# Kernel optimization log

Measured on AMD Instinct MI355X. Metric: run time of the kernel, lower is better.

## Reference

```python
import jax, jax.numpy as jnp
import numpy as np

B_SZ, L_SEQ, D_DATA = 2, 1024, 8
D_CTRL = 256
POLY = 40
N_LAYERS = 2
D_STATE = 16
D_CONV = 4
D_INNER = 1 * D_CTRL          # expand_factor_control = 1
DT_RANK = -(-D_CTRL // 16)    # ceil(d_model/16) = 16
EPS = 1e-5


def setup_inputs() -> dict:
    key = jax.random.key(0)
    ks = jax.random.split(key, 12)
    s = 0.02
    x = jax.random.uniform(ks[0], (B_SZ, L_SEQ, D_DATA), dtype=jnp.float32)
    y = jax.random.uniform(ks[1], (B_SZ, L_SEQ, D_DATA), dtype=jnp.float32)
    return {
        'x': x,
        'y': y,
        # control_proj (note: fed 2*d_data features in structured forward)
        'control_proj_w': jax.random.normal(ks[2], (D_CTRL, 2 * D_DATA)) * s,
        'control_proj_b': jnp.zeros((D_CTRL,), jnp.float32),
        # stacked Mamba layer params (leading dim = n_layers)
        'norm_w': jnp.ones((N_LAYERS, D_CTRL), jnp.float32),
        'in_proj_w': jax.random.normal(ks[3], (N_LAYERS, 2 * D_INNER, D_CTRL)) * s,
        'conv_w': jax.random.normal(ks[4], (N_LAYERS, D_INNER, D_CONV)) * s,
        'conv_b': jnp.zeros((N_LAYERS, D_INNER), jnp.float32),
        'x_proj_w': jax.random.normal(ks[5], (N_LAYERS, DT_RANK + 2 * D_STATE, D_INNER)) * s,
        'dt_proj_w': jax.random.normal(ks[6], (N_LAYERS, D_INNER, DT_RANK)) * s,
        'dt_proj_b': jnp.zeros((N_LAYERS, D_INNER), jnp.float32),
        'A_log': jnp.tile(jnp.log(jnp.arange(1, D_STATE + 1, dtype=jnp.float32))[None, None, :], (N_LAYERS, D_INNER, 1)),
        'D_skip': jnp.ones((N_LAYERS, D_INNER), jnp.float32),
        'out_proj_w': jax.random.normal(ks[7], (N_LAYERS, D_CTRL, D_INNER)) * s,
        # b_net: Linear(d_control, 2*d_data*poly_dim^2)
        'b_net_w': jax.random.normal(ks[8], (2 * D_DATA * POLY * POLY, D_CTRL)) * s,
        'b_net_b': jnp.zeros((2 * D_DATA * POLY * POLY,), jnp.float32),
    }


def _rmsnorm(u, w):
    return u * jax.lax.rsqrt(jnp.mean(u * u, axis=-1, keepdims=True) + EPS) * w


def _causal_conv(u, w, b):
    # u: [B,L,C]; w: [C,K] depthwise causal conv, pad left K-1
    K = w.shape[-1]
    L = u.shape[1]
    up = jnp.pad(u, ((0, 0), (K - 1, 0), (0, 0)))
    acc = jnp.zeros_like(u)
    for k in range(K):  # K=4, fixed small kernel
        acc = acc + up[:, k:k + L, :] * w[:, k]
    return acc + b


def _mamba(u, norm_w, in_proj_w, conv_w, conv_b, x_proj_w, dt_proj_w, dt_proj_b, A_log, D_skip, out_proj_w):
    # mambapy-style stack of residual blocks: u = mixer(rmsnorm(u)) + u
    for i in range(N_LAYERS):
        r = _rmsnorm(u, norm_w[i])
        xz = jnp.einsum('bld,ed->ble', r, in_proj_w[i])          # [B,L,2*di]
        xc, zg = jnp.split(xz, 2, axis=-1)
        xc = jax.nn.silu(_causal_conv(xc, conv_w[i], conv_b[i]))  # [B,L,di]
        dbc = jnp.einsum('bld,ed->ble', xc, x_proj_w[i])          # [B,L,dt_rank+2*ds]
        delta = jax.nn.softplus(jnp.einsum('blr,dr->bld', dbc[..., :DT_RANK], dt_proj_w[i]) + dt_proj_b[i])
        Bm = dbc[..., DT_RANK:DT_RANK + D_STATE]
        Cm = dbc[..., DT_RANK + D_STATE:]
        A = -jnp.exp(A_log[i])                                    # [di,ds]
        dA = jnp.exp(delta[..., None] * A)                        # [B,L,di,ds]
        dBx = delta[..., None] * Bm[:, :, None, :] * xc[..., None]

        def step(h, inp):
            dA_t, dBx_t = inp
            h = dA_t * h + dBx_t
            return h, h

        h0 = jnp.zeros((u.shape[0], D_INNER, D_STATE), u.dtype)
        _, hs = jax.lax.scan(step, h0, (dA.transpose(1, 0, 2, 3), dBx.transpose(1, 0, 2, 3)))
        yv = jnp.einsum('lbds,lbs->bld', hs, Cm.transpose(1, 0, 2)) + D_skip[i] * xc
        yv = yv * jax.nn.silu(zg)
        u = jnp.einsum('bld,ed->ble', yv, out_proj_w[i]) + u
    return u


def _power_mat(z):
    # z ** arange(POLY), built with cumprod (grad-safe at exponent 0)
    ones = jnp.ones(z.shape + (1,), z.dtype)
    reps = jnp.broadcast_to(z[..., None], z.shape + (POLY - 1,))
    return jnp.cumprod(jnp.concatenate([ones, reps], axis=-1), axis=-1)  # [B,L,2d,P]


def reference(x, y, control_proj_w, control_proj_b, norm_w, in_proj_w, conv_w, conv_b,
              x_proj_w, dt_proj_w, dt_proj_b, A_log, D_skip, out_proj_w, b_net_w, b_net_b):
    B, L, d = x.shape
    xdot = y - x
    z = jnp.concatenate([x, xdot], axis=-1)                       # [B,L,2d]
    pm = _power_mat(z)                                            # [B,L,2d,P]
    ctrl_in = jnp.flip(jnp.concatenate([xdot, y], axis=-1), axis=1)
    ctrl_in = ctrl_in @ control_proj_w.T + control_proj_b
    sp = _mamba(ctrl_in, norm_w, in_proj_w, conv_w, conv_b, x_proj_w,
                dt_proj_w, dt_proj_b, A_log, D_skip, out_proj_w)
    state_pred = jnp.flip(sp, axis=1)                             # [B,L,d_ctrl]
    bmat = (state_pred @ b_net_w.T + b_net_b).reshape(B, L, 2 * d, POLY, POLY)
    pow1 = jnp.einsum('bldkj,bldk->bldj', bmat, pm)
    zdot = jnp.einsum('bldj,bldj->bld', pow1, jnp.flip(pm, axis=2))
    return zdot[:, 1:, :], state_pred
```

## Files before the change

kernel.cpp:

```cpp
#include <hip/hip_runtime.h>
#include <hip/hip_bf16.h>

#define B_SZ   2
#define LSEQ   1024
#define DD     8
#define DCTRL  256
#define POLY   40
#define NL     2
#define DSTATE 16
#define DCONV  4
#define DINNER 256
#define DTRANK 16
#define NBL    (B_SZ*LSEQ)
#define NROWS  (2*DD*POLY*POLY)
#define NSLOT  25
#define NCH    32
#define LCH    32

typedef __attribute__((ext_vector_type(8))) short bf16x8;
typedef __attribute__((ext_vector_type(8))) unsigned short us8;
typedef __attribute__((ext_vector_type(4))) unsigned short us4;
typedef __attribute__((ext_vector_type(4))) float f32x4;

__device__ __forceinline__ float sigmoidf_(float x){ return 1.f/(1.f+__expf(-x)); }
__device__ __forceinline__ float softplusf_(float x){ return fmaxf(x,0.f) + log1pf(__expf(-fabsf(x))); }
__device__ __forceinline__ unsigned short f2bf(float f){
  unsigned int u = __float_as_uint(f);
  unsigned int r = (u + 0x7fffu + ((u>>16)&1u)) >> 16;
  return (unsigned short)r;
}

__global__ void k_f2bf(const float* __restrict__ in, unsigned short* __restrict__ out, int n8){
  int i = blockIdx.x*blockDim.x + threadIdx.x;
  if (i>=n8) return;
  const float4* p = (const float4*)(in + (size_t)i*8);
  float4 a = p[0], b = p[1];
  us8 r;
  r[0]=f2bf(a.x); r[1]=f2bf(a.y); r[2]=f2bf(a.z); r[3]=f2bf(a.w);
  r[4]=f2bf(b.x); r[5]=f2bf(b.y); r[6]=f2bf(b.z); r[7]=f2bf(b.w);
  *(us8*)(out + (size_t)i*8) = r;
}

#define IPW_N8 (NL*512*256/8)
#define OPW_N8 (NL*256*256/8)
#define PRE_B0 ((IPW_N8+OPW_N8)/256)
#define PRE_B1 (NL*288*256/256)
#define PRE_B2 (16*NBL/256)
#define PRE_B3 (NBL*256/256)
#define PRE_B4 (NROWS*256/8/256)
__global__ void k_prologue(const float* __restrict__ ipw, const float* __restrict__ opw,
                           const float* __restrict__ dtw, const float* __restrict__ xpw,
                           const float* __restrict__ x,   const float* __restrict__ y,
                           const float* __restrict__ cpw, const float* __restrict__ cpb,
                           const float* __restrict__ bnw,
                           unsigned short* __restrict__ ipwb,
                           unsigned short* __restrict__ wcomb,
                           float* __restrict__ pmt, float* __restrict__ u,
                           unsigned short* __restrict__ Wb){
  int bx = blockIdx.x; int tid = threadIdx.x;
  if (bx < PRE_B0){
    int i = bx*256 + tid;
    const float* src = (i < IPW_N8) ? (ipw + (size_t)i*8) : (opw + (size_t)(i-IPW_N8)*8);
    const float4* p = (const float4*)src;
    float4 a = p[0], b = p[1];
    us8 r;
    r[0]=f2bf(a.x); r[1]=f2bf(a.y); r[2]=f2bf(a.z); r[3]=f2bf(a.w);
    r[4]=f2bf(b.x); r[5]=f2bf(b.y); r[6]=f2bf(b.z); r[7]=f2bf(b.w);
    *(us8*)(ipwb + (size_t)i*8) = r;
  } else if (bx < PRE_B0+PRE_B1){
    int idx = (bx-PRE_B0)*256 + tid;
    int e = idx & 255; int row = (idx>>8) % 288; int l = idx / (288*256);
    float v;
    if (row < 256){
      float s=0.f;
      #pragma unroll
      for (int r=0;r<16;++r) s += dtw[((size_t)l*256+row)*16+r] * xpw[((size_t)l*48+r)*256+e];
      v = s;
    } else {
      v = xpw[((size_t)l*48 + (row-240))*256 + e];
    }
    wcomb[idx] = f2bf(v);
  } else if (bx < PRE_B0+PRE_B1+PRE_B2){
    int idx = (bx-PRE_B0-PRE_B1)*256 + tid;
    int m = idx & (NBL-1); int c = idx >> 11;
    float z;
    if (c < 8) z = x[(size_t)m*8 + c];
    else       z = y[(size_t)m*8 + (c-8)] - x[(size_t)m*8 + (c-8)];
    float p = 1.f;
    #pragma unroll
    for (int j=0;j<POLY;++j){ pmt[((size_t)c*POLY+j)*NBL + m] = p; p*=z; }
  } else if (bx < PRE_B0+PRE_B1+PRE_B2+PRE_B3){
    int idx = (bx-PRE_B0-PRE_B1-PRE_B2)*256 + tid;
    int e = idx & 255; int m = idx >> 8;
    int bb = m >> 10; int lm = m & 1023; int lo = 1023 - lm;
    const float* xp = x + ((size_t)bb*1024+lo)*8;
    const float* yp = y + ((size_t)bb*1024+lo)*8;
    const float* wr = cpw + (size_t)e*16;
    float acc = cpb[e];
    #pragma unroll
    for (int d=0; d<8; ++d) acc += (yp[d]-xp[d])*wr[d];
    #pragma unroll
    for (int d=0; d<8; ++d) acc += yp[d]*wr[8+d];
    u[idx] = acc;
  } else {
    int i = (bx-PRE_B0-PRE_B1-PRE_B2-PRE_B3)*256 + tid;
    const float4* p = (const float4*)(bnw + (size_t)i*8);
    float4 a = p[0], b = p[1];
    us8 r;
    r[0]=f2bf(a.x); r[1]=f2bf(a.y); r[2]=f2bf(a.z); r[3]=f2bf(a.w);
    r[4]=f2bf(b.x); r[5]=f2bf(b.y); r[6]=f2bf(b.z); r[7]=f2bf(b.w);
    *(us8*)(Wb + (size_t)i*8) = r;
  }
}

__global__ void k_rms(const float* __restrict__ u, const float* __restrict__ nw,
                      unsigned short* __restrict__ rb){
  int m = blockIdx.x; int e = threadIdx.x;
  float v = u[(size_t)m*256 + e];
  float ss = v*v;
  #pragma unroll
  for (int off=32; off>0; off>>=1) ss += __shfl_down(ss, off);
  __shared__ float sred[4];
  __shared__ float srstd;
  int wid = e>>6; int lane = e&63;
  if (lane==0) sred[wid]=ss;
  __syncthreads();
  if (e==0){ float t = sred[0]+sred[1]+sred[2]+sred[3]; srstd = rsqrtf(t*(1.f/256.f) + 1e-5f); }
  __syncthreads();
  rb[(size_t)m*256+e] = f2bf(v * srstd * nw[e]);
}

__global__ void __launch_bounds__(256)
gemm_bf(const unsigned short* __restrict__ A, const unsigned short* __restrict__ B,
        int N, int K, const float* __restrict__ bias,
        float* __restrict__ C0, float* __restrict__ C1, int ldc, int mode,
        float* __restrict__ outsp, unsigned short* __restrict__ spb){
  __shared__ __align__(16) unsigned short Asm[64*40];
  __shared__ __align__(16) unsigned short Bsm[64*40];
  int tid = threadIdx.x;
  int lane = tid & 63;
  int w = tid >> 6; int wr = w >> 1, wc = w & 1;
  int l15 = lane & 15, l4 = lane >> 4;
  int m0 = blockIdx.y*64, n0 = blockIdx.x*64;

  f32x4 acc[2][2];
  #pragma unroll
  for (int i=0;i<2;++i)
    #pragma unroll
    for (int j=0;j<2;++j){ acc[i][j][0]=0.f; acc[i][j][1]=0.f; acc[i][j][2]=0.f; acc[i][j][3]=0.f; }

  int row = tid>>2, c8 = tid&3;
  int nks = K >> 5;
  for (int ks=0; ks<nks; ++ks){
    int k0 = ks*32;
    *(us8*)&Asm[row*40 + c8*8] = *(const us8*)(A + (size_t)(m0+row)*K + k0 + c8*8);
    {
      int bn = n0+row;
      us8 v;
      if (bn < N){
        v = *(const us8*)(B + (size_t)bn*K + k0 + c8*8);
      } else {
        for (int z=0;z<8;++z) v[z]=0;
      }
      *(us8*)&Bsm[row*40 + c8*8] = v;
    }
    __syncthreads();
    bf16x8 av[2], bv[2];
    #pragma unroll
    for (int i=0;i<2;++i) av[i] = *(bf16x8*)&Asm[(wr*32+i*16+l15)*40 + l4*8];
    #pragma unroll
    for (int j=0;j<2;++j) bv[j] = *(bf16x8*)&Bsm[(wc*32+j*16+l15)*40 + l4*8];
    #pragma unroll
    for (int i=0;i<2;++i)
      #pragma unroll
      for (int j=0;j<2;++j)
        acc[i][j] = __builtin_amdgcn_mfma_f32_16x16x32_bf16(av[i], bv[j], acc[i][j], 0,0,0);
    __syncthreads();
  }

  #pragma unroll
  for (int i=0;i<2;++i){
    #pragma unroll
    for (int j=0;j<2;++j){
      int n = n0 + wc*32 + j*16 + l15;
      #pragma unroll
      for (int q=0;q<4;++q){
        int m = m0 + wr*32 + i*16 + l4*4 + q;
        float v = acc[i][j][q];
        if (mode==0){
          C0[(size_t)m*ldc + n] = v;
        } else if (mode==1){
          C0[(size_t)m*ldc + n] += v;
        } else if (mode==2){
          if (n < 256) C0[(size_t)m*256 + n] = softplusf_(v + bias[n]);
          else if (n < N) C1[(size_t)m*32 + (n-256)] = v;
        } else {
          float t = C0[(size_t)m*ldc + n] + v;
          int bb = m >> 10; int lq = m & 1023;
          size_t mf = (size_t)bb*1024 + (1023-lq);
          outsp[mf*256 + n] = t;
          spb[mf*256 + n] = f2bf(t);
        }
      }
    }
  }
}

__global__ void k_convsilu(const float* __restrict__ xz, const float* __restrict__ cw,
                           const float* __restrict__ cb, float* __restrict__ xc,
                           unsigned short* __restrict__ xcb){
  int idx = blockIdx.x*blockDim.x + threadIdx.x;
  if (idx >= NBL*64) return;
  int d4 = (idx & 63) << 2; int m = idx >> 6;
  int bb = m>>10, l = m&1023;
  float4 w0 = *(const float4*)&cw[(d4+0)*4];
  float4 w1 = *(const float4*)&cw[(d4+1)*4];
  float4 w2 = *(const float4*)&cw[(d4+2)*4];
  float4 w3 = *(const float4*)&cw[(d4+3)*4];
  float4 cbv = *(const float4*)&cb[d4];
  float a0=cbv.x, a1=cbv.y, a2=cbv.z, a3=cbv.w;
  #pragma unroll
  for (int k=0;k<4;++k){
    int ls = l - 3 + k;
    if (ls >= 0){
      float4 v = *(const float4*)&xz[((size_t)(bb*1024+ls))*512 + d4];
      a0 += v.x * ((const float*)&w0)[k];
      a1 += v.y * ((const float*)&w1)[k];
      a2 += v.z * ((const float*)&w2)[k];
      a3 += v.w * ((const float*)&w3)[k];
    }
  }
  a0 = a0*sigmoidf_(a0); a1 = a1*sigmoidf_(a1);
  a2 = a2*sigmoidf_(a2); a3 = a3*sigmoidf_(a3);
  float4 o; o.x=a0; o.y=a1; o.z=a2; o.w=a3;
  *(float4*)&xc[(size_t)m*256 + d4] = o;
  us4 ob; ob[0]=f2bf(a0); ob[1]=f2bf(a1); ob[2]=f2bf(a2); ob[3]=f2bf(a3);
  *(us4*)&xcb[(size_t)m*256 + d4] = ob;
}

__global__ void k_scan1(const float* __restrict__ delta, const float* __restrict__ bc,
                        const float* __restrict__ xc, const float* __restrict__ alog,
                        float* __restrict__ hend, float* __restrict__ Pc){
  int blk = blockIdx.x;
  int dg = blk & 15; int ch = (blk>>4) & (NCH-1); int bb = blk >> 9;
  int tid = threadIdx.x; int dl = tid>>4; int s = tid&15; int d = dg*16+dl;
  float A = -__expf(alog[(size_t)d*16+s]);
  float h = 0.f, p = 1.f;
  size_t base = (size_t)bb*1024 + ch*LCH;
  #pragma unroll 4
  for (int t=0;t<LCH;++t){
    size_t mb = base + t;
    float de  = delta[mb*256+d];
    float Bv  = bc[mb*32+s];
    float xcv = xc[mb*256+d];
    float a = __expf(de*A);
    h = a*h + de*Bv*xcv;
    p *= a;
  }
  size_t o = (((size_t)bb*NCH+ch)*256+d)*16+s;
  hend[o]=h; Pc[o]=p;
}

__global__ void k_scan2(const float* __restrict__ hend, const float* __restrict__ Pc,
                        float* __restrict__ Hinit){
  int idx = blockIdx.x*blockDim.x + threadIdx.x;
  if (idx >= B_SZ*256*16) return;
  int bb = idx >> 12; int ds = idx & 4095;
  float H = 0.f;
  #pragma unroll
  for (int ch=0; ch<NCH; ++ch){
    size_t o = ((size_t)bb*NCH+ch)*4096 + ds;
    Hinit[o] = H;
    H = Pc[o]*H + hend[o];
  }
}

__global__ void k_scan3(const float* __restrict__ delta, const float* __restrict__ bc,
                        const float* __restrict__ xc, const float* __restrict__ xz,
                        const float* __restrict__ alog, const float* __restrict__ dskip,
                        const float* __restrict__ Hinit, unsigned short* __restrict__ yvb){
  int blk = blockIdx.x;
  int dg = blk & 15; int ch = (blk>>4) & (NCH-1); int bb = blk >> 9;
  int tid = threadIdx.x; int dl = tid>>4; int s = tid&15; int d = dg*16+dl;
  float A = -__expf(alog[(size_t)d*16+s]);
  float dsk = dskip[d];
  float h = Hinit[(((size_t)bb*NCH+ch)*256+d)*16+s];
  size_t base = (size_t)bb*1024 + ch*LCH;
  #pragma unroll 2
  for (int t=0;t<LCH;++t){
    size_t mb = base + t;
    float de  = delta[mb*256+d];
    float Bv  = bc[mb*32+s];
    float Cv  = bc[mb*32+16+s];
    float xcv = xc[mb*256+d];
    float a = __expf(de*A);
    h = a*h + de*Bv*xcv;
    float yval = h*Cv;
    yval += __shfl_xor(yval,1);
    yval += __shfl_xor(yval,2);
    yval += __shfl_xor(yval,4);
    yval += __shfl_xor(yval,8);
    if (s==0){
      float zg = xz[mb*512+256+d];
      yvb[mb*256+d] = f2bf((yval + dsk*xcv) * zg * sigmoidf_(zg));
    }
  }
}

__global__ void __launch_bounds__(512)
k_bnet_mfma(const unsigned short* __restrict__ spb, const unsigned short* __restrict__ Wb,
            const float* __restrict__ bnb, const float* __restrict__ pmt,
            float* __restrict__ part){
  __shared__ __align__(16) unsigned short Asm[2][256*40];
  __shared__ __align__(16) unsigned short Bsm[2][64*40];
  __shared__ float red[2][256];

  int tid = threadIdx.x;
  int lane = tid & 63;
  int w = tid >> 6;
  int wr = w >> 1, wc = w & 1;
  int l15 = lane & 15, l4 = lane >> 4;
  int bx = blockIdx.x;
  int m0 = blockIdx.y*256;
  int n0 = bx*64;

  int aRow0 = (tid)>>2,        aC0 = (tid)&3;
  int aRow1 = (tid+512)>>2,    aC1 = (tid+512)&3;
  int bRow  = tid>>2,          bC  = tid&3;
  const unsigned short* aSrc0 = spb + ((size_t)(m0+aRow0))*256 + aC0*8;
  const unsigned short* aSrc1 = spb + ((size_t)(m0+aRow1))*256 + aC1*8;
  const unsigned short* bSrc  = Wb  + ((size_t)(n0+bRow ))*256 + bC*8;

  f32x4 acc[4][2];
  #pragma unroll
  for (int i=0;i<4;++i)
    #pragma unroll
    for (int j=0;j<2;++j){ acc[i][j][0]=0.f; acc[i][j][1]=0.f; acc[i][j][2]=0.f; acc[i][j][3]=0.f; }

  us8 rA0 = *(const us8*)(aSrc0);
  us8 rA1 = *(const us8*)(aSrc1);
  us8 rB;
  if (tid < 256) rB = *(const us8*)(bSrc);
  *(us8*)&Asm[0][aRow0*40 + aC0*8] = rA0;
  *(us8*)&Asm[0][aRow1*40 + aC1*8] = rA1;
  if (tid < 256) *(us8*)&Bsm[0][bRow*40 + bC*8] = rB;
  __syncthreads();

  int cur = 0;
  for (int ks=0; ks<8; ++ks){
    if (ks < 7){
      int k0n = (ks+1)*32;
      rA0 = *(const us8*)(aSrc0 + k0n);
      rA1 = *(const us8*)(aSrc1 + k0n);
      if (tid < 256) rB = *(const us8*)(bSrc + k0n);
    }
    bf16x8 av[4], bv[2];
    #pragma unroll
    for (int i=0;i<4;++i) av[i] = *(bf16x8*)&Asm[cur][(wr*64+i*16+l15)*40 + l4*8];
    #pragma unroll
    for (int j=0;j<2;++j) bv[j] = *(bf16x8*)&Bsm[cur][(wc*32+j*16+l15)*40 + l4*8];
    __builtin_amdgcn_s_setprio(1);
    #pragma unroll
    for (int i=0;i<4;++i)
      #pragma unroll
      for (int j=0;j<2;++j)
        acc[i][j] = __builtin_amdgcn_mfma_f32_16x16x32_bf16(av[i], bv[j], acc[i][j], 0,0,0);
    __builtin_amdgcn_s_setprio(0);
    if (ks < 7){
      *(us8*)&Asm[cur^1][aRow0*40 + aC0*8] = rA0;
      *(us8*)&Asm[cur^1][aRow1*40 + aC1*8] = rA1;
      if (tid < 256) *(us8*)&Bsm[cur^1][bRow*40 + bC*8] = rB;
    }
    __syncthreads();
    cur ^= 1;
  }

  int c = bx/25, slot = bx%25;
  int rem0 = slot*64;
  float bnbv[2]; int kkv[2], jjv[2];
  #pragma unroll
  for (int j=0;j<2;++j){
    int nl = wc*32 + j*16 + l15;
    int rem = rem0 + nl;
    bnbv[j] = bnb[n0 + nl];
    kkv[j] = rem/40; jjv[j] = rem%40;
  }
  const float* pc  = pmt + (size_t)c*POLY*NBL;
  const float* pcf = pmt + (size_t)(15-c)*POLY*NBL;
  #pragma unroll
  for (int i=0;i<4;++i){
    int mb = m0 + wr*64 + i*16 + l4*4;
    f32x4 s; s[0]=0.f; s[1]=0.f; s[2]=0.f; s[3]=0.f;
    #pragma unroll
    for (int j=0;j<2;++j){
      f32x4 pk = *(const f32x4*)&pc [(size_t)kkv[j]*NBL + mb];
      f32x4 pj = *(const f32x4*)&pcf[(size_t)jjv[j]*NBL + mb];
      #pragma unroll
      for (int q=0;q<4;++q) s[q] += (acc[i][j][q] + bnbv[j]) * pk[q] * pj[q];
    }
    #pragma unroll
    for (int q=0;q<4;++q){
      float t = s[q];
      t += __shfl_xor(t,1); t += __shfl_xor(t,2);
      t += __shfl_xor(t,4); t += __shfl_xor(t,8);
      if (l15==0) red[wc][wr*64 + i*16 + l4*4 + q] = t;
    }
  }
  __syncthreads();
  if (tid < 256){
    float v = red[0][tid] + red[1][tid];
    part[((size_t)(c*NSLOT + slot))*NBL + m0 + tid] = v;
  }
}

__global__ void k_final(const float* __restrict__ part, float* __restrict__ out){
  int j = blockIdx.x*blockDim.x+threadIdx.x;
  if (j >= 16*2046) return;
  int c = j / 2046; int r = j % 2046;
  int bb = r / 1023; int l = r % 1023 + 1;
  size_t m = (size_t)bb*1024 + l;
  float s = 0.f;
  #pragma unroll
  for (int q=0;q<NSLOT;++q) s += part[((size_t)(c*NSLOT + q))*NBL + m];
  out[((size_t)(bb*1023 + (l-1)))*16 + c] = s;
}

extern "C" void kernel_launch(void* const* d_in, const int* in_sizes, int n_in,
                              void* d_out, int out_size, void* d_ws, size_t ws_size,
                              hipStream_t stream) {
  const float* x    = (const float*)d_in[0];
  const float* y    = (const float*)d_in[1];
  const float* cpw  = (const float*)d_in[2];
  const float* cpb  = (const float*)d_in[3];
  const float* nw   = (const float*)d_in[4];
  const float* ipw  = (const float*)d_in[5];
  const float* cvw  = (const float*)d_in[6];
  const float* cvb  = (const float*)d_in[7];
  const float* xpw  = (const float*)d_in[8];
  const float* dtw  = (const float*)d_in[9];
  const float* dtb  = (const float*)d_in[10];
  const float* alog = (const float*)d_in[11];
  const float* dsk  = (const float*)d_in[12];
  const float* opw  = (const float*)d_in[13];
  const float* bnw  = (const float*)d_in[14];
  const float* bnb  = (const float*)d_in[15];

  float* out      = (float*)d_out;
  float* out_zdot = out;
  float* out_sp   = out + 32736;

  float* ws = (float*)d_ws;
  size_t off = 0;
  float* u     = ws + off; off += (size_t)NBL*256;
  unsigned short* rb = (unsigned short*)(ws + off); off += (size_t)NBL*256/2;
  float* xz    = ws + off; off += (size_t)NBL*512;
  float* xc    = ws + off; off += (size_t)NBL*256;
  unsigned short* xcb = (unsigned short*)(ws + off); off += (size_t)NBL*256/2;
  float* delta = ws + off; off += (size_t)NBL*256;
  float* bcm   = ws + off; off += (size_t)NBL*32;
  unsigned short* yvb = (unsigned short*)(ws + off); off += (size_t)NBL*256/2;
  float* pmt   = ws + off; off += (size_t)NBL*16*POLY;
  float* part  = ws + off; off += (size_t)NSLOT*NBL*16;
  float* hend  = ws + off; off += (size_t)B_SZ*NCH*256*16;
  float* Pc    = ws + off; off += (size_t)B_SZ*NCH*256*16;
  float* Hinit = ws + off; off += (size_t)B_SZ*NCH*256*16;
  unsigned short* spb  = (unsigned short*)(ws + off); off += (size_t)NBL*256/2;
  unsigned short* ipwb = (unsigned short*)(ws + off); off += (size_t)(IPW_N8+OPW_N8)*4;
  unsigned short* wcomb= (unsigned short*)(ws + off); off += (size_t)NL*288*256/2;

  int wbEarly = ((off + (size_t)NROWS*256/2)*sizeof(float) <= ws_size) ? 1 : 0;
  unsigned short* Wb = wbEarly ? (unsigned short*)(ws + off) : (unsigned short*)ws;

  unsigned short* opwb = ipwb + (size_t)IPW_N8*8;

  int preBlocks = PRE_B0+PRE_B1+PRE_B2+PRE_B3 + (wbEarly ? PRE_B4 : 0);
  k_prologue<<<preBlocks, 256, 0, stream>>>(ipw, opw, dtw, xpw, x, y, cpw, cpb, bnw,
                                            ipwb, wcomb, pmt, u, Wb);

  for (int i=0;i<NL;++i){
    k_rms<<<NBL, 256, 0, stream>>>(u, nw + i*256, rb);
    gemm_bf<<<dim3(8,32), 256, 0, stream>>>(rb, ipwb + (size_t)i*512*256, 512, 256,
                                            nullptr, xz, nullptr, 512, 0, nullptr, nullptr);
    k_convsilu<<<(NBL*64+255)/256, 256, 0, stream>>>(xz, cvw + i*256*4, cvb + i*256, xc, xcb);
    gemm_bf<<<dim3(5,32), 256, 0, stream>>>(xcb, wcomb + (size_t)i*288*256, 288, 256,
                                            dtb + i*256, delta, bcm, 256, 2, nullptr, nullptr);
    k_scan1<<<B_SZ*NCH*16, 256, 0, stream>>>(delta, bcm, xc, alog + (size_t)i*256*16, hend, Pc);
    k_scan2<<<(B_SZ*256*16+255)/256, 256, 0, stream>>>(hend, Pc, Hinit);
    k_scan3<<<B_SZ*NCH*16, 256, 0, stream>>>(delta, bcm, xc, xz, alog + (size_t)i*256*16,
                                             dsk + i*256, Hinit, yvb);
    if (i < NL-1){
      gemm_bf<<<dim3(4,32), 256, 0, stream>>>(yvb, opwb + (size_t)i*256*256, 256, 256,
                                              nullptr, u, nullptr, 256, 1, nullptr, nullptr);
    } else {
      gemm_bf<<<dim3(4,32), 256, 0, stream>>>(yvb, opwb + (size_t)i*256*256, 256, 256,
                                              nullptr, u, nullptr, 256, 3, out_sp, spb);
    }
  }

  if (!wbEarly){
    k_f2bf<<<(NROWS*256/8 + 255)/256, 256, 0, stream>>>(bnw, Wb, NROWS*256/8);
  }
  k_bnet_mfma<<<dim3(NROWS/64, NBL/256), 512, 0, stream>>>(spb, Wb, bnb, pmt, part);
  k_final<<<(16*2046+255)/256, 256, 0, stream>>>(part, out_zdot);
}
```

Measured before the change: 229.3 us.

## Fold chunk-prefix scan into scan3 and shrink LDS row stride to 36

The separate k_scan2 launch and its Hinit buffer are removed. Each k_scan3 block now recomputes its own starting state by serially combining the end states and decay products of all earlier chunks, which trades one kernel launch and one global round-trip for redundant prefix work (up to 31 steps per thread). The shared-memory row padding in both MFMA GEMMs is also changed from 40 to 36 bf16 elements, intended to change the LDS bank-conflict pattern and reduce shared-memory footprint.

```diff
diff --git a/kernel.cpp b/kernel.cpp
--- a/kernel.cpp
+++ b/kernel.cpp
@@ -16,6 +16,7 @@
 #define NSLOT  25
 #define NCH    32
 #define LCH    32
+#define LDP    36
 
 typedef __attribute__((ext_vector_type(8))) short bf16x8;
 typedef __attribute__((ext_vector_type(8))) unsigned short us8;
@@ -135,8 +136,8 @@
         int N, int K, const float* __restrict__ bias,
         float* __restrict__ C0, float* __restrict__ C1, int ldc, int mode,
         float* __restrict__ outsp, unsigned short* __restrict__ spb){
-  __shared__ __align__(16) unsigned short Asm[64*40];
-  __shared__ __align__(16) unsigned short Bsm[64*40];
+  __shared__ __align__(16) unsigned short Asm[64*LDP];
+  __shared__ __align__(16) unsigned short Bsm[64*LDP];
   int tid = threadIdx.x;
   int lane = tid & 63;
   int w = tid >> 6; int wr = w >> 1, wc = w & 1;
@@ -153,7 +154,7 @@
   int nks = K >> 5;
   for (int ks=0; ks<nks; ++ks){
     int k0 = ks*32;
-    *(us8*)&Asm[row*40 + c8*8] = *(const us8*)(A + (size_t)(m0+row)*K + k0 + c8*8);
+    *(us8*)&Asm[row*LDP + c8*8] = *(const us8*)(A + (size_t)(m0+row)*K + k0 + c8*8);
     {
       int bn = n0+row;
       us8 v;
@@ -162,14 +163,14 @@
       } else {
         for (int z=0;z<8;++z) v[z]=0;
       }
-      *(us8*)&Bsm[row*40 + c8*8] = v;
+      *(us8*)&Bsm[row*LDP + c8*8] = v;
     }
     __syncthreads();
     bf16x8 av[2], bv[2];
     #pragma unroll
-    for (int i=0;i<2;++i) av[i] = *(bf16x8*)&Asm[(wr*32+i*16+l15)*40 + l4*8];
-    #pragma unroll
-    for (int j=0;j<2;++j) bv[j] = *(bf16x8*)&Bsm[(wc*32+j*16+l15)*40 + l4*8];
+    for (int i=0;i<2;++i) av[i] = *(bf16x8*)&Asm[(wr*32+i*16+l15)*LDP + l4*8];
+    #pragma unroll
+    for (int j=0;j<2;++j) bv[j] = *(bf16x8*)&Bsm[(wc*32+j*16+l15)*LDP + l4*8];
     #pragma unroll
     for (int i=0;i<2;++i)
       #pragma unroll
@@ -261,30 +262,22 @@
   hend[o]=h; Pc[o]=p;
 }
 
-__global__ void k_scan2(const float* __restrict__ hend, const float* __restrict__ Pc,
-                        float* __restrict__ Hinit){
-  int idx = blockIdx.x*blockDim.x + threadIdx.x;
-  if (idx >= B_SZ*256*16) return;
-  int bb = idx >> 12; int ds = idx & 4095;
-  float H = 0.f;
-  #pragma unroll
-  for (int ch=0; ch<NCH; ++ch){
-    size_t o = ((size_t)bb*NCH+ch)*4096 + ds;
-    Hinit[o] = H;
-    H = Pc[o]*H + hend[o];
-  }
-}
-
 __global__ void k_scan3(const float* __restrict__ delta, const float* __restrict__ bc,
                         const float* __restrict__ xc, const float* __restrict__ xz,
                         const float* __restrict__ alog, const float* __restrict__ dskip,
-                        const float* __restrict__ Hinit, unsigned short* __restrict__ yvb){
+                        const float* __restrict__ hend, const float* __restrict__ Pc,
+                        unsigned short* __restrict__ yvb){
   int blk = blockIdx.x;
   int dg = blk & 15; int ch = (blk>>4) & (NCH-1); int bb = blk >> 9;
   int tid = threadIdx.x; int dl = tid>>4; int s = tid&15; int d = dg*16+dl;
   float A = -__expf(alog[(size_t)d*16+s]);
   float dsk = dskip[d];
-  float h = Hinit[(((size_t)bb*NCH+ch)*256+d)*16+s];
+  float h = 0.f;
+  size_t dso = (size_t)d*16 + s;
+  for (int cc=0; cc<ch; ++cc){
+    size_t o = ((size_t)bb*NCH+cc)*4096 + dso;
+    h = Pc[o]*h + hend[o];
+  }
   size_t base = (size_t)bb*1024 + ch*LCH;
   #pragma unroll 2
   for (int t=0;t<LCH;++t){
@@ -311,8 +304,8 @@
 k_bnet_mfma(const unsigned short* __restrict__ spb, const unsigned short* __restrict__ Wb,
             const float* __restrict__ bnb, const float* __restrict__ pmt,
             float* __restrict__ part){
-  __shared__ __align__(16) unsigned short Asm[2][256*40];
-  __shared__ __align__(16) unsigned short Bsm[2][64*40];
+  __shared__ __align__(16) unsigned short Asm[2][256*LDP];
+  __shared__ __align__(16) unsigned short Bsm[2][64*LDP];
   __shared__ float red[2][256];
 
   int tid = threadIdx.x;
@@ -341,9 +334,9 @@
   us8 rA1 = *(const us8*)(aSrc1);
   us8 rB;
   if (tid < 256) rB = *(const us8*)(bSrc);
-  *(us8*)&Asm[0][aRow0*40 + aC0*8] = rA0;
-  *(us8*)&Asm[0][aRow1*40 + aC1*8] = rA1;
-  if (tid < 256) *(us8*)&Bsm[0][bRow*40 + bC*8] = rB;
+  *(us8*)&Asm[0][aRow0*LDP + aC0*8] = rA0;
+  *(us8*)&Asm[0][aRow1*LDP + aC1*8] = rA1;
+  if (tid < 256) *(us8*)&Bsm[0][bRow*LDP + bC*8] = rB;
   __syncthreads();
 
   int cur = 0;
@@ -356,9 +349,9 @@
     }
     bf16x8 av[4], bv[2];
     #pragma unroll
-    for (int i=0;i<4;++i) av[i] = *(bf16x8*)&Asm[cur][(wr*64+i*16+l15)*40 + l4*8];
-    #pragma unroll
-    for (int j=0;j<2;++j) bv[j] = *(bf16x8*)&Bsm[cur][(wc*32+j*16+l15)*40 + l4*8];
+    for (int i=0;i<4;++i) av[i] = *(bf16x8*)&Asm[cur][(wr*64+i*16+l15)*LDP + l4*8];
+    #pragma unroll
+    for (int j=0;j<2;++j) bv[j] = *(bf16x8*)&Bsm[cur][(wc*32+j*16+l15)*LDP + l4*8];
     __builtin_amdgcn_s_setprio(1);
     #pragma unroll
     for (int i=0;i<4;++i)
@@ -367,9 +360,9 @@
         acc[i][j] = __builtin_amdgcn_mfma_f32_16x16x32_bf16(av[i], bv[j], acc[i][j], 0,0,0);
     __builtin_amdgcn_s_setprio(0);
     if (ks < 7){
-      *(us8*)&Asm[cur^1][aRow0*40 + aC0*8] = rA0;
-      *(us8*)&Asm[cur^1][aRow1*40 + aC1*8] = rA1;
-      if (tid < 256) *(us8*)&Bsm[cur^1][bRow*40 + bC*8] = rB;
+      *(us8*)&Asm[cur^1][aRow0*LDP + aC0*8] = rA0;
+      *(us8*)&Asm[cur^1][aRow1*LDP + aC1*8] = rA1;
+      if (tid < 256) *(us8*)&Bsm[cur^1][bRow*LDP + bC*8] = rB;
     }
     __syncthreads();
     cur ^= 1;
@@ -463,7 +456,6 @@
   float* part  = ws + off; off += (size_t)NSLOT*NBL*16;
   float* hend  = ws + off; off += (size_t)B_SZ*NCH*256*16;
   float* Pc    = ws + off; off += (size_t)B_SZ*NCH*256*16;
-  float* Hinit = ws + off; off += (size_t)B_SZ*NCH*256*16;
   unsigned short* spb  = (unsigned short*)(ws + off); off += (size_t)NBL*256/2;
   unsigned short* ipwb = (unsigned short*)(ws + off); off += (size_t)(IPW_N8+OPW_N8)*4;
   unsigned short* wcomb= (unsigned short*)(ws + off); off += (size_t)NL*288*256/2;
@@ -485,9 +477,8 @@
     gemm_bf<<<dim3(5,32), 256, 0, stream>>>(xcb, wcomb + (size_t)i*288*256, 288, 256,
                                             dtb + i*256, delta, bcm, 256, 2, nullptr, nullptr);
     k_scan1<<<B_SZ*NCH*16, 256, 0, stream>>>(delta, bcm, xc, alog + (size_t)i*256*16, hend, Pc);
-    k_scan2<<<(B_SZ*256*16+255)/256, 256, 0, stream>>>(hend, Pc, Hinit);
     k_scan3<<<B_SZ*NCH*16, 256, 0, stream>>>(delta, bcm, xc, xz, alog + (size_t)i*256*16,
-                                             dsk + i*256, Hinit, yvb);
+                                             dsk + i*256, hend, Pc, yvb);
     if (i < NL-1){
       gemm_bf<<<dim3(4,32), 256, 0, stream>>>(yvb, opwb + (size_t)i*256*256, 256, 256,
                                               nullptr, u, nullptr, 256, 1, nullptr, nullptr);
```

After: 242.8 us. 1.06x slower.

## Load b_net MFMA operands directly from global, drop LDS staging

Applied to the files above, without the earlier changes.

The b_net GEMM kernel no longer stages A and B tiles through double-buffered shared memory. Each lane now loads its MFMA fragments straight from global memory into registers, prefetching the next k-step, and the per-iteration barriers go away. The block shrinks from 512 to 256 threads with a 128-row M tile, which doubles the grid. This removes LDS traffic and synchronisation but loses cross-wave reuse, so each wave re-reads operands from global/L2 and global load traffic rises.

```diff
diff --git a/kernel.cpp b/kernel.cpp
--- a/kernel.cpp
+++ b/kernel.cpp
@@ -16,6 +16,7 @@
 #define NSLOT  25
 #define NCH    32
 #define LCH    32
+#define LDP    40
 
 typedef __attribute__((ext_vector_type(8))) short bf16x8;
 typedef __attribute__((ext_vector_type(8))) unsigned short us8;
@@ -135,8 +136,8 @@
         int N, int K, const float* __restrict__ bias,
         float* __restrict__ C0, float* __restrict__ C1, int ldc, int mode,
         float* __restrict__ outsp, unsigned short* __restrict__ spb){
-  __shared__ __align__(16) unsigned short Asm[64*40];
-  __shared__ __align__(16) unsigned short Bsm[64*40];
+  __shared__ __align__(16) unsigned short Asm[64*LDP];
+  __shared__ __align__(16) unsigned short Bsm[64*LDP];
   int tid = threadIdx.x;
   int lane = tid & 63;
   int w = tid >> 6; int wr = w >> 1, wc = w & 1;
@@ -153,7 +154,7 @@
   int nks = K >> 5;
   for (int ks=0; ks<nks; ++ks){
     int k0 = ks*32;
-    *(us8*)&Asm[row*40 + c8*8] = *(const us8*)(A + (size_t)(m0+row)*K + k0 + c8*8);
+    *(us8*)&Asm[row*LDP + c8*8] = *(const us8*)(A + (size_t)(m0+row)*K + k0 + c8*8);
     {
       int bn = n0+row;
       us8 v;
@@ -162,14 +163,14 @@
       } else {
         for (int z=0;z<8;++z) v[z]=0;
       }
-      *(us8*)&Bsm[row*40 + c8*8] = v;
+      *(us8*)&Bsm[row*LDP + c8*8] = v;
     }
     __syncthreads();
     bf16x8 av[2], bv[2];
     #pragma unroll
-    for (int i=0;i<2;++i) av[i] = *(bf16x8*)&Asm[(wr*32+i*16+l15)*40 + l4*8];
-    #pragma unroll
-    for (int j=0;j<2;++j) bv[j] = *(bf16x8*)&Bsm[(wc*32+j*16+l15)*40 + l4*8];
+    for (int i=0;i<2;++i) av[i] = *(bf16x8*)&Asm[(wr*32+i*16+l15)*LDP + l4*8];
+    #pragma unroll
+    for (int j=0;j<2;++j) bv[j] = *(bf16x8*)&Bsm[(wc*32+j*16+l15)*LDP + l4*8];
     #pragma unroll
     for (int i=0;i<2;++i)
       #pragma unroll
@@ -307,13 +308,11 @@
   }
 }
 
-__global__ void __launch_bounds__(512)
+__global__ void __launch_bounds__(256)
 k_bnet_mfma(const unsigned short* __restrict__ spb, const unsigned short* __restrict__ Wb,
             const float* __restrict__ bnb, const float* __restrict__ pmt,
             float* __restrict__ part){
-  __shared__ __align__(16) unsigned short Asm[2][256*40];
-  __shared__ __align__(16) unsigned short Bsm[2][64*40];
-  __shared__ float red[2][256];
+  __shared__ float red[2][128];
 
   int tid = threadIdx.x;
   int lane = tid & 63;
@@ -321,15 +320,15 @@
   int wr = w >> 1, wc = w & 1;
   int l15 = lane & 15, l4 = lane >> 4;
   int bx = blockIdx.x;
-  int m0 = blockIdx.y*256;
+  int m0 = blockIdx.y*128;
   int n0 = bx*64;
 
-  int aRow0 = (tid)>>2,        aC0 = (tid)&3;
-  int aRow1 = (tid+512)>>2,    aC1 = (tid+512)&3;
-  int bRow  = tid>>2,          bC  = tid&3;
-  const unsigned short* aSrc0 = spb + ((size_t)(m0+aRow0))*256 + aC0*8;
-  const unsigned short* aSrc1 = spb + ((size_t)(m0+aRow1))*256 + aC1*8;
-  const unsigned short* bSrc  = Wb  + ((size_t)(n0+bRow ))*256 + bC*8;
+  const unsigned short* aP[4];
+  const unsigned short* bP[2];
+  #pragma unroll
+  for (int i=0;i<4;++i) aP[i] = spb + (size_t)(m0 + wr*64 + i*16 + l15)*256 + l4*8;
+  #pragma unroll
+  for (int j=0;j<2;++j) bP[j] = Wb  + (size_t)(n0 + wc*32 + j*16 + l15)*256 + l4*8;
 
   f32x4 acc[4][2];
   #pragma unroll
@@ -337,28 +336,21 @@
     #pragma unroll
     for (int j=0;j<2;++j){ acc[i][j][0]=0.f; acc[i][j][1]=0.f; acc[i][j][2]=0.f; acc[i][j][3]=0.f; }
 
-  us8 rA0 = *(const us8*)(aSrc0);
-  us8 rA1 = *(const us8*)(aSrc1);
-  us8 rB;
-  if (tid < 256) rB = *(const us8*)(bSrc);
-  *(us8*)&Asm[0][aRow0*40 + aC0*8] = rA0;
-  *(us8*)&Asm[0][aRow1*40 + aC1*8] = rA1;
-  if (tid < 256) *(us8*)&Bsm[0][bRow*40 + bC*8] = rB;
-  __syncthreads();
-
-  int cur = 0;
+  bf16x8 av[4], bv[2], avn[4], bvn[2];
+  #pragma unroll
+  for (int i=0;i<4;++i) av[i] = *(const bf16x8*)(aP[i]);
+  #pragma unroll
+  for (int j=0;j<2;++j) bv[j] = *(const bf16x8*)(bP[j]);
+
+  #pragma unroll
   for (int ks=0; ks<8; ++ks){
     if (ks < 7){
       int k0n = (ks+1)*32;
-      rA0 = *(const us8*)(aSrc0 + k0n);
-      rA1 = *(const us8*)(aSrc1 + k0n);
-      if (tid < 256) rB = *(const us8*)(bSrc + k0n);
-    }
-    bf16x8 av[4], bv[2];
-    #pragma unroll
-    for (int i=0;i<4;++i) av[i] = *(bf16x8*)&Asm[cur][(wr*64+i*16+l15)*40 + l4*8];
-    #pragma unroll
-    for (int j=0;j<2;++j) bv[j] = *(bf16x8*)&Bsm[cur][(wc*32+j*16+l15)*40 + l4*8];
+      #pragma unroll
+      for (int i=0;i<4;++i) avn[i] = *(const bf16x8*)(aP[i] + k0n);
+      #pragma unroll
+      for (int j=0;j<2;++j) bvn[j] = *(const bf16x8*)(bP[j] + k0n);
+    }
     __builtin_amdgcn_s_setprio(1);
     #pragma unroll
     for (int i=0;i<4;++i)
@@ -367,12 +359,11 @@
         acc[i][j] = __builtin_amdgcn_mfma_f32_16x16x32_bf16(av[i], bv[j], acc[i][j], 0,0,0);
     __builtin_amdgcn_s_setprio(0);
     if (ks < 7){
-      *(us8*)&Asm[cur^1][aRow0*40 + aC0*8] = rA0;
-      *(us8*)&Asm[cur^1][aRow1*40 + aC1*8] = rA1;
-      if (tid < 256) *(us8*)&Bsm[cur^1][bRow*40 + bC*8] = rB;
-    }
-    __syncthreads();
-    cur ^= 1;
+      #pragma unroll
+      for (int i=0;i<4;++i) av[i] = avn[i];
+      #pragma unroll
+      for (int j=0;j<2;++j) bv[j] = bvn[j];
+    }
   }
 
   int c = bx/25, slot = bx%25;
@@ -407,7 +398,7 @@
     }
   }
   __syncthreads();
-  if (tid < 256){
+  if (tid < 128){
     float v = red[0][tid] + red[1][tid];
     part[((size_t)(c*NSLOT + slot))*NBL + m0 + tid] = v;
   }
@@ -500,6 +491,6 @@
   if (!wbEarly){
     k_f2bf<<<(NROWS*256/8 + 255)/256, 256, 0, stream>>>(bnw, Wb, NROWS*256/8);
   }
-  k_bnet_mfma<<<dim3(NROWS/64, NBL/256), 512, 0, stream>>>(spb, Wb, bnb, pmt, part);
+  k_bnet_mfma<<<dim3(NROWS/64, NBL/128), 256, 0, stream>>>(spb, Wb, bnb, pmt, part);
   k_final<<<(16*2046+255)/256, 256, 0, stream>>>(part, out_zdot);
 }
```

New measurement: 319.1 us. +39.2%, slower.
